# Performance work log

Hardware: AMD Instinct MI355X
Metric: run time of the kernel (lower is better)

Reference implementation:

```python
import jax, jax.numpy as jnp
from jax import lax
import numpy as np

N = 4
ALPHA_AP = 0.85
ALPHA_DS = 0.1
ALPHA_LR = 1.0
C1 = 0.01 ** 2
C2 = 0.03 ** 2


def resize_ac(img, nh, nw):
    # bilinear resize, align_corners=True (matches F.interpolate(..., align_corners=True))
    B, C, H, W = img.shape
    ys = jnp.linspace(0.0, H - 1.0, nh)
    xs = jnp.linspace(0.0, W - 1.0, nw)
    y0 = jnp.floor(ys).astype(jnp.int32)
    y1 = jnp.minimum(y0 + 1, H - 1)
    x0 = jnp.floor(xs).astype(jnp.int32)
    x1 = jnp.minimum(x0 + 1, W - 1)
    wy = (ys - y0).astype(img.dtype)[None, None, :, None]
    wx = (xs - x0).astype(img.dtype)[None, None, None, :]
    top = img[:, :, y0, :] * (1.0 - wy) + img[:, :, y1, :] * wy
    return top[:, :, :, x0] * (1.0 - wx) + top[:, :, :, x1] * wx


def build_pyramid(img):
    B, C, H, W = img.shape
    pyr = [img]
    for i in range(N - 1):
        r = 2 ** (i + 1)
        pyr.append(resize_ac(pyr[i], H // r, W // r))  # resize previous level, as in torch code
    return pyr


def x_grad(img):
    # replicate-pad right then diff -> last column is exactly zero
    g = img[:, :, :, :-1] - img[:, :, :, 1:]
    return jnp.concatenate([g, jnp.zeros_like(img[:, :, :, :1])], axis=3)


def y_grad(img):
    g = img[:, :, :-1, :] - img[:, :, 1:, :]
    return jnp.concatenate([g, jnp.zeros_like(img[:, :, :1, :])], axis=2)


def avgpool3(x):
    # AvgPool2d(3, 1), VALID padding
    return lax.reduce_window(x, 0.0, lax.add, (1, 1, 3, 3), (1, 1, 1, 1), 'VALID') / 9.0


def grid_sample_zeros(img, gx, gy):
    # bilinear grid_sample, padding_mode='zeros', align_corners=True
    B, C, H, W = img.shape
    x = (gx + 1.0) * 0.5 * (W - 1)
    y = (gy + 1.0) * 0.5 * (H - 1)
    x0 = jnp.floor(x)
    y0 = jnp.floor(y)

    def corner(xi, yi, w):
        valid = (xi >= 0) & (xi <= W - 1) & (yi >= 0) & (yi <= H - 1)
        xc = jnp.clip(xi, 0, W - 1).astype(jnp.int32)
        yc = jnp.clip(yi, 0, H - 1).astype(jnp.int32)
        vals = jax.vmap(lambda im, yy, xx: im[:, yy, xx])(img, yc, xc)  # [B,C,H,W]
        return vals * (w * valid.astype(img.dtype))[:, None]

    return (corner(x0, y0, (x0 + 1 - x) * (y0 + 1 - y))
            + corner(x0 + 1, y0, (x - x0) * (y0 + 1 - y))
            + corner(x0, y0 + 1, (x0 + 1 - x) * (y - y0))
            + corner(x0 + 1, y0 + 1, (x - x0) * (y - y0)))


def apply_disparity(img, disp):
    # standard Monodepth bilinear sampler: shift x_base in [0,1] by disp, grid_sample
    B, C, H, W = img.shape
    x_base = jnp.linspace(0.0, 1.0, W)[None, None, :]
    y_base = jnp.linspace(0.0, 1.0, H)[None, :, None]
    gx = 2.0 * (x_base + disp[:, 0]) - 1.0  # [B,H,W]
    gy = jnp.broadcast_to(2.0 * y_base - 1.0, gx.shape)
    return grid_sample_zeros(img, gx, gy)


def dssim(x, y):
    mu_x = avgpool3(x)
    mu_y = avgpool3(y)
    sig_x = avgpool3(x * x) - mu_x ** 2
    sig_y = avgpool3(y * y) - mu_y ** 2
    cov = avgpool3(x * y) - mu_x * mu_y
    ssim = ((2.0 * mu_x * mu_y + C1) * (2.0 * cov + C2)) / ((mu_x ** 2 + mu_y ** 2 + C1) * (sig_x + sig_y + C2))
    return jnp.mean(jnp.clip((1.0 - ssim) / 2.0, 0.0, 1.0))


def smoothness(disp, img, level):
    wx = jnp.exp(-jnp.mean(jnp.abs(x_grad(img)), axis=1, keepdims=True))
    wy = jnp.exp(-jnp.mean(jnp.abs(y_grad(img)), axis=1, keepdims=True))
    sx = x_grad(disp) * wx
    sy = y_grad(disp) * wy
    return jnp.mean(jnp.abs(sx) + jnp.abs(sy)) / (2 ** level)


def loss_forward(disps, left, right):
    lp = build_pyramid(left)
    rp = build_pyramid(right)
    dl = [d[:, 0:1] for d in disps]
    dr = [d[:, 1:2] for d in disps]
    left_est = [apply_disparity(rp[i], -dl[i]) for i in range(N)]
    right_est = [apply_disparity(lp[i], dr[i]) for i in range(N)]
    r2l_disp = [apply_disparity(dr[i], -dl[i]) for i in range(N)]
    l2r_disp = [apply_disparity(dl[i], dr[i]) for i in range(N)]
    # appearance matching (note: outer *ALPHA_AP matches the original's AP_loss*self.alpha_AP)
    AP = sum(ALPHA_AP * dssim(lp[i], left_est[i]) + (1.0 - ALPHA_AP) * jnp.mean(jnp.abs(lp[i] - left_est[i])) for i in range(N))
    AP = AP + sum(ALPHA_AP * dssim(rp[i], right_est[i]) + (1.0 - ALPHA_AP) * jnp.mean(jnp.abs(rp[i] - right_est[i])) for i in range(N))
    AP = AP * ALPHA_AP
    LR = sum(jnp.mean(jnp.abs(dl[i] - r2l_disp[i])) for i in range(N))
    LR = (LR + sum(jnp.mean(jnp.abs(dr[i] - l2r_disp[i])) for i in range(N))) * ALPHA_LR
    DS = sum(smoothness(dl[i], lp[i], i) for i in range(N))
    DS = (DS + sum(smoothness(dr[i], rp[i], i) for i in range(N))) * ALPHA_DS
    total = AP + LR + DS
    return total, AP, LR, DS


def setup_inputs() -> dict:
    key = jax.random.key(0)
    ks = jax.random.split(key, 6)
    B, H, W = 32, 256, 512
    inp = {}
    for i in range(N):
        h, w = H >> i, W >> i
        # normalized disparities in [0, 0.05) as in trained Monodepth
        inp[f'disp{i}'] = jax.random.uniform(ks[i], (B, 2, h, w), jnp.float32) * 0.05
    inp['left'] = jax.random.uniform(ks[4], (B, 3, H, W), jnp.float32)
    inp['right'] = jax.random.uniform(ks[5], (B, 3, H, W), jnp.float32)
    return inp


def reference(disp0, disp1, disp2, disp3, left, right):
    return loss_forward([disp0, disp1, disp2, disp3], left, right)
```

## Files before the change

### kernel.cpp

```cpp
#include <hip/hip_runtime.h>

#define BDIM 256
#define SH 16

struct LevelDesc {
    const float* lp; const float* rp; const float* dp;
    int H, W, nCW, nRS, nPerSide, waveBase;
};
struct AllParams { LevelDesc lv[4]; int totalWaves; };

__global__ void zero_acc_kernel(double* acc) {
    if (threadIdx.x < 32) acc[threadIdx.x] = 0.0;
}

__global__ void resize2_kernel(const float* __restrict__ sL, const float* __restrict__ sR,
                               float* __restrict__ dL, float* __restrict__ dR,
                               int BC, int Hs, int Ws, int Hd, int Wd) {
    long long half = (long long)BC * Hd * Wd;
    long long idx = (long long)blockIdx.x * blockDim.x + threadIdx.x;
    if (idx >= 2 * half) return;
    const float* src = (idx < half) ? sL : sR;
    float* dst = (idx < half) ? dL : dR;
    long long id = (idx < half) ? idx : idx - half;
    int i = (int)(id % Wd);
    long long t = id / Wd;
    int j = (int)(t % Hd);
    int bc = (int)(t / Hd);
    float stepy = (float)(Hs - 1) / (float)(Hd - 1);
    float stepx = (float)(Ws - 1) / (float)(Wd - 1);
    float y = j * stepy;
    float x = i * stepx;
    int y0 = (int)floorf(y);
    int y1 = min(y0 + 1, Hs - 1);
    int x0 = (int)floorf(x);
    int x1 = min(x0 + 1, Ws - 1);
    float wy = y - (float)y0;
    float wx = x - (float)x0;
    const float* s = src + (long long)bc * Hs * Ws;
    float t0 = s[(long long)y0 * Ws + x0] * (1.0f - wy) + s[(long long)y1 * Ws + x0] * wy;
    float t1 = s[(long long)y0 * Ws + x1] * (1.0f - wy) + s[(long long)y1 * Ws + x1] * wy;
    dst[id] = t0 * (1.0f - wx) + t1 * wx;
}

__device__ __forceinline__ float ssim_term(float Sx, float Sy, float Sxx, float Syy, float Sxy) {
    const float C1v = 0.0001f;
    const float C2v = 0.0009f;
    float mux = Sx * (1.0f / 9.0f), muy = Sy * (1.0f / 9.0f);
    float sigx = Sxx * (1.0f / 9.0f) - mux * mux;
    float sigy = Syy * (1.0f / 9.0f) - muy * muy;
    float cov  = Sxy * (1.0f / 9.0f) - mux * muy;
    float num = (2.0f * mux * muy + C1v) * (2.0f * cov + C2v);
    float den = (mux * mux + muy * muy + C1v) * (sigx + sigy + C2v);
    float v = (1.0f - num * __builtin_amdgcn_rcpf(den)) * 0.5f;
    return fminf(fmaxf(v, 0.0f), 1.0f);
}

__global__ void __launch_bounds__(BDIM)
mega_kernel(AllParams P, double* __restrict__ acc) {
    const int lane = threadIdx.x & 63;
    const int wid  = threadIdx.x >> 6;
    const int wId  = blockIdx.x * (BDIM / 64) + wid;
    const int w = min(wId, P.totalWaves - 1);

    int level = 0;
    if (w >= P.lv[1].waveBase) level = 1;
    if (w >= P.lv[2].waveBase) level = 2;
    if (w >= P.lv[3].waveBase) level = 3;
    LevelDesc L;
    if (level == 0) L = P.lv[0];
    else if (level == 1) L = P.lv[1];
    else if (level == 2) L = P.lv[2];
    else L = P.lv[3];

    int rel = w - L.waveBase;
    const int side = (rel >= L.nPerSide) ? 1 : 0;
    rel -= side * L.nPerSide;
    const int cw = rel % L.nCW; rel /= L.nCW;
    const int rs = rel % L.nRS;
    const int b  = rel / L.nRS;

    const int H = L.H, W = L.W;
    const long long HW = (long long)H * W;
    const float Wm1f = (float)(W - 1);
    const float sgn = side ? 1.0f : -1.0f;

    const float* xim = (side ? L.rp : L.lp) + (long long)b * 3 * HW;
    const float* sim = (side ? L.lp : L.rp) + (long long)b * 3 * HW;
    const float* dme = L.dp + (long long)b * 2 * HW + (side ? HW : 0);
    const float* dot = L.dp + (long long)b * 2 * HW + (side ? 0 : HW);

    const int base = cw * 126;
    const int c0 = base + 2 * lane;
    const int c1 = c0 + 1;
    const bool in0 = c0 < W, in1 = c1 < W;
    const int cc = min(c0, W - 2) >> 1;
    const float fc0 = (float)c0, fc1 = (float)c1;

    const bool lastW = (cw == L.nCW - 1);
    const bool own0 = in0 && (c0 < base + 126 || lastW);
    const bool own1 = in1 && (c1 < base + 126 || lastW);
    const bool ownS0 = own0 && (c0 <= W - 3);
    const bool ownS1 = own1 && (c1 <= W - 3);

    const int r0 = rs * SH;
    const int r1 = min(r0 + SH, H);
    const int jend = min(r1 + 1, H - 1);

    float Pst[3][5][2], Lst[3][5][2];
#pragma unroll
    for (int c = 0; c < 3; ++c)
#pragma unroll
        for (int s = 0; s < 5; ++s) { Pst[c][s][0] = 0.f; Pst[c][s][1] = 0.f;
                                      Lst[c][s][0] = 0.f; Lst[c][s][1] = 0.f; }
    float pd0 = 0.f, pd1 = 0.f;
    float pxv[3][2] = {{0.f,0.f},{0.f,0.f},{0.f,0.f}};

    float f_ss = 0.f, f_l1 = 0.f, f_lr = 0.f, f_ds = 0.f;

    for (int j = r0; j <= jend; ++j) {
        const long long ro = (long long)j * W;
        float2 dpair = ((const float2*)(dme + ro))[cc];
        float d0 = dpair.x, d1 = dpair.y;

        float xq0 = fmaf(sgn * d0, Wm1f, fc0);
        float xq1 = fmaf(sgn * d1, Wm1f, fc1);
        float xf0 = floorf(xq0), xf1 = floorf(xq1);
        int g0 = (int)xf0, g1 = (int)xf1;
        float t0 = xq0 - xf0, t1 = xq1 - xf1;
        float w00 = (g0 >= 0 && g0 < W)         ? 1.0f - t0 : 0.0f;
        float w01 = (g0 >= -1 && g0 < W - 1)    ? t0        : 0.0f;
        float w10 = (g1 >= 0 && g1 < W)         ? 1.0f - t1 : 0.0f;
        float w11 = (g1 >= -1 && g1 < W - 1)    ? t1        : 0.0f;
        int a0 = min(max(g0, 0), W - 1);
        int a1 = min(max(g0 + 1, 0), W - 1);
        int b0 = min(max(g1, 0), W - 1);
        int b1 = min(max(g1 + 1, 0), W - 1);

        const float* dor = dot + ro;
        float wv0 = dor[a0] * w00 + dor[a1] * w01;
        float wv1 = dor[b0] * w10 + dor[b1] * w11;

        float xv[3][2], yv[3][2];
#pragma unroll
        for (int c = 0; c < 3; ++c) {
            const float* xr = xim + (long long)c * HW + ro;
            const float* sr = sim + (long long)c * HW + ro;
            float2 xp2 = ((const float2*)xr)[cc];
            xv[c][0] = in0 ? xp2.x : 0.f;
            xv[c][1] = in1 ? xp2.y : 0.f;
            yv[c][0] = sr[a0] * w00 + sr[a1] * w01;
            yv[c][1] = sr[b0] * w10 + sr[b1] * w11;
            if (!in0) yv[c][0] = 0.f;
            if (!in1) yv[c][1] = 0.f;
        }

        const bool rowOwn = j < r1;
        if (rowOwn) {
            if (own0) {
                f_l1 += fabsf(xv[0][0] - yv[0][0]) + fabsf(xv[1][0] - yv[1][0]) + fabsf(xv[2][0] - yv[2][0]);
                f_lr += fabsf(d0 - wv0);
            }
            if (own1) {
                f_l1 += fabsf(xv[0][1] - yv[0][1]) + fabsf(xv[1][1] - yv[1][1]) + fabsf(xv[2][1] - yv[2][1]);
                f_lr += fabsf(d1 - wv1);
            }
        }

        {
            float dn  = __shfl_down(d0, 1);
            float xn0 = __shfl_down(xv[0][0], 1);
            float xn1 = __shfl_down(xv[1][0], 1);
            float xn2 = __shfl_down(xv[2][0], 1);
            if (rowOwn) {
                if (own0 && c0 < W - 1) {
                    float g = fabsf(xv[0][0] - xv[0][1]) + fabsf(xv[1][0] - xv[1][1]) + fabsf(xv[2][0] - xv[2][1]);
                    f_ds += fabsf((d0 - d1) * __expf(-g * (1.0f / 3.0f)));
                }
                if (own1 && c1 < W - 1) {
                    float g = fabsf(xv[0][1] - xn0) + fabsf(xv[1][1] - xn1) + fabsf(xv[2][1] - xn2);
                    f_ds += fabsf((d1 - dn) * __expf(-g * (1.0f / 3.0f)));
                }
            }
        }
        if (j > r0 && (j - 1) < r1) {
            if (own0) {
                float g = fabsf(pxv[0][0] - xv[0][0]) + fabsf(pxv[1][0] - xv[1][0]) + fabsf(pxv[2][0] - xv[2][0]);
                f_ds += fabsf((pd0 - d0) * __expf(-g * (1.0f / 3.0f)));
            }
            if (own1) {
                float g = fabsf(pxv[0][1] - xv[0][1]) + fabsf(pxv[1][1] - xv[1][1]) + fabsf(pxv[2][1] - xv[2][1]);
                f_ds += fabsf((pd1 - d1) * __expf(-g * (1.0f / 3.0f)));
            }
        }
        pd0 = d0; pd1 = d1;
#pragma unroll
        for (int c = 0; c < 3; ++c) { pxv[c][0] = xv[c][0]; pxv[c][1] = xv[c][1]; }

        const bool emit = (j >= r0 + 2);
#pragma unroll
        for (int c = 0; c < 3; ++c) {
            float cs[5][2];
#pragma unroll
            for (int p = 0; p < 2; ++p) {
                float cx = xv[c][p], cy = yv[c][p];
                float v5[5] = {cx, cy, cx * cx, cy * cy, cx * cy};
#pragma unroll
                for (int s = 0; s < 5; ++s) {
                    cs[s][p] = Pst[c][s][p] + v5[s];
                    Pst[c][s][p] = Lst[c][s][p] + v5[s];
                    Lst[c][s][p] = v5[s];
                }
            }
            if (emit) {
                float w0s[5], w1s[5];
#pragma unroll
                for (int s = 0; s < 5; ++s) {
                    float n0 = __shfl_down(cs[s][0], 1);
                    float n1 = __shfl_down(cs[s][1], 1);
                    w0s[s] = cs[s][0] + cs[s][1] + n0;
                    w1s[s] = cs[s][1] + n0 + n1;
                }
                float ts0 = ssim_term(w0s[0], w0s[1], w0s[2], w0s[3], w0s[4]);
                float ts1 = ssim_term(w1s[0], w1s[1], w1s[2], w1s[3], w1s[4]);
                f_ss += (ownS0 ? ts0 : 0.f) + (ownS1 ? ts1 : 0.f);
            }
        }
    }

#pragma unroll
    for (int o = 32; o > 0; o >>= 1) {
        f_ss += __shfl_down(f_ss, o);
        f_l1 += __shfl_down(f_l1, o);
        f_lr += __shfl_down(f_lr, o);
        f_ds += __shfl_down(f_ds, o);
    }
    __shared__ float red[BDIM / 64][4];
    __shared__ int meta[2];
    if (threadIdx.x == 0) { meta[0] = level; meta[1] = side; }
    if (lane == 0) {
        red[wid][0] = f_ss; red[wid][1] = f_l1;
        red[wid][2] = f_lr; red[wid][3] = f_ds;
    }
    __syncthreads();
    if (threadIdx.x < 4) {
        int t = threadIdx.x;
        double s = (double)red[0][t] + (double)red[1][t]
                 + (double)red[2][t] + (double)red[3][t];
        atomicAdd(acc + t * 8 + meta[1] * 4 + meta[0], s);
    }
}

__global__ void finalize_kernel(const double* __restrict__ acc, float* __restrict__ out) {
    const int B = 32, H0 = 256, W0 = 512;
    double AP = 0.0, LR = 0.0, DS = 0.0;
    for (int i = 0; i < 4; ++i) {
        int h = H0 >> i, w = W0 >> i;
        double nss = (double)B * 3.0 * (double)(h - 2) * (double)(w - 2);
        double nl1 = (double)B * 3.0 * (double)h * (double)w;
        double nd  = (double)B * (double)h * (double)w;
        AP += 0.85 * (acc[0 + i] / nss) + 0.15 * (acc[8 + i] / nl1);
        AP += 0.85 * (acc[4 + i] / nss) + 0.15 * (acc[12 + i] / nl1);
        LR += acc[16 + i] / nd + acc[20 + i] / nd;
        double sc = 1.0 / (double)(1 << i);
        DS += (acc[24 + i] / nd) * sc + (acc[28 + i] / nd) * sc;
    }
    AP *= 0.85;
    DS *= 0.1;
    double total = AP + LR + DS;
    out[0] = (float)total;
    out[1] = (float)AP;
    out[2] = (float)LR;
    out[3] = (float)DS;
}

extern "C" void kernel_launch(void* const* d_in, const int* in_sizes, int n_in,
                              void* d_out, int out_size, void* d_ws, size_t ws_size,
                              hipStream_t stream) {
    const int B = 32, H0 = 256, W0 = 512;
    const float* dsp[4];
    for (int i = 0; i < 4; ++i) dsp[i] = (const float*)d_in[i];
    const float* left  = (const float*)d_in[4];
    const float* right = (const float*)d_in[5];
    float* out = (float*)d_out;

    double* acc = (double*)d_ws;
    float* buf = (float*)((char*)d_ws + 256);

    const float* lp[4];
    const float* rp[4];
    float* lpm[4];
    float* rpm[4];
    lp[0] = left; rp[0] = right;
    float* cur = buf;
    for (int i = 1; i < 4; ++i) { lpm[i] = cur; cur += (long long)B * 3 * (H0 >> i) * (W0 >> i); }
    for (int i = 1; i < 4; ++i) { rpm[i] = cur; cur += (long long)B * 3 * (H0 >> i) * (W0 >> i); }
    for (int i = 1; i < 4; ++i) { lp[i] = lpm[i]; rp[i] = rpm[i]; }

    zero_acc_kernel<<<1, 64, 0, stream>>>(acc);

    for (int i = 1; i < 4; ++i) {
        int Hs = H0 >> (i - 1), Ws = W0 >> (i - 1);
        int Hd = H0 >> i, Wd = W0 >> i;
        long long half = (long long)B * 3 * Hd * Wd;
        int g = (int)((2 * half + BDIM - 1) / BDIM);
        resize2_kernel<<<g, BDIM, 0, stream>>>(
            lp[i - 1], rp[i - 1], lpm[i], rpm[i], B * 3, Hs, Ws, Hd, Wd);
    }

    AllParams P;
    int wb = 0;
    for (int i = 0; i < 4; ++i) {
        int h = H0 >> i, w = W0 >> i;
        LevelDesc& L = P.lv[i];
        L.lp = lp[i]; L.rp = rp[i]; L.dp = dsp[i];
        L.H = h; L.W = w;
        L.nCW = (w - 2 + 125) / 126;
        L.nRS = h / SH;
        L.nPerSide = B * L.nRS * L.nCW;
        L.waveBase = wb;
        wb += 2 * L.nPerSide;
    }
    P.totalWaves = wb;
    int blocks = (wb + (BDIM / 64) - 1) / (BDIM / 64);
    mega_kernel<<<blocks, BDIM, 0, stream>>>(P, acc);

    finalize_kernel<<<1, 1, 0, stream>>>(acc, out);
}
```

Before: 301.7 us.

## Fuse resize, loss and finalize into one persistent kernel with grid barriers

Merges the three pyramid resize launches, the main loss kernel and the finalize kernel into a single persistent kernel of 1280 blocks. Stages are separated by atomic-counter grid barriers. The row split per wave is rebalanced so each wave handles H/nChunks rows, with exactly 5120 waves. This removes launch overhead and tail effects, but relies on all 1280 blocks being co-resident (launch bounds request 5 blocks per CU), otherwise the spin barrier deadlocks. It also hardcodes the wave partition per level.

```diff
diff --git a/kernel.cpp b/kernel.cpp
--- a/kernel.cpp
+++ b/kernel.cpp
@@ -1,45 +1,63 @@
 #include <hip/hip_runtime.h>
 
 #define BDIM 256
-#define SH 16
+#define GRID 1280
+#define NWAVES (GRID * (BDIM / 64))
 
 struct LevelDesc {
     const float* lp; const float* rp; const float* dp;
-    int H, W, nCW, nRS, nPerSide, waveBase;
+    int H, W, nCW, nChunks, base, nPerSide;
 };
-struct AllParams { LevelDesc lv[4]; int totalWaves; };
-
-__global__ void zero_acc_kernel(double* acc) {
+struct Params {
+    LevelDesc lv[4];
+    const float* left; const float* right;
+    float* l1; float* r1; float* l2; float* r2; float* l3; float* r3;
+    double* acc; unsigned int* cnt; float* out;
+};
+
+__global__ void init_kernel(double* acc, unsigned int* cnt) {
     if (threadIdx.x < 32) acc[threadIdx.x] = 0.0;
-}
-
-__global__ void resize2_kernel(const float* __restrict__ sL, const float* __restrict__ sR,
-                               float* __restrict__ dL, float* __restrict__ dR,
-                               int BC, int Hs, int Ws, int Hd, int Wd) {
-    long long half = (long long)BC * Hd * Wd;
-    long long idx = (long long)blockIdx.x * blockDim.x + threadIdx.x;
-    if (idx >= 2 * half) return;
-    const float* src = (idx < half) ? sL : sR;
-    float* dst = (idx < half) ? dL : dR;
-    long long id = (idx < half) ? idx : idx - half;
-    int i = (int)(id % Wd);
-    long long t = id / Wd;
-    int j = (int)(t % Hd);
-    int bc = (int)(t / Hd);
-    float stepy = (float)(Hs - 1) / (float)(Hd - 1);
-    float stepx = (float)(Ws - 1) / (float)(Wd - 1);
-    float y = j * stepy;
-    float x = i * stepx;
-    int y0 = (int)floorf(y);
-    int y1 = min(y0 + 1, Hs - 1);
-    int x0 = (int)floorf(x);
-    int x1 = min(x0 + 1, Ws - 1);
-    float wy = y - (float)y0;
-    float wx = x - (float)x0;
-    const float* s = src + (long long)bc * Hs * Ws;
-    float t0 = s[(long long)y0 * Ws + x0] * (1.0f - wy) + s[(long long)y1 * Ws + x0] * wy;
-    float t1 = s[(long long)y0 * Ws + x1] * (1.0f - wy) + s[(long long)y1 * Ws + x1] * wy;
-    dst[id] = t0 * (1.0f - wx) + t1 * wx;
+    else if (threadIdx.x == 32) *cnt = 0u;
+}
+
+__device__ __forceinline__ void gsync(unsigned int* cnt, unsigned int target) {
+    __syncthreads();
+    if (threadIdx.x == 0) {
+        __threadfence();
+        atomicAdd(cnt, 1u);
+        while (atomicAdd(cnt, 0u) < target) __builtin_amdgcn_s_sleep(2);
+        __threadfence();
+    }
+    __syncthreads();
+}
+
+__device__ void resize_dev(const float* __restrict__ sL, const float* __restrict__ sR,
+                           float* __restrict__ dL, float* __restrict__ dR,
+                           int BC, int Hs, int Ws, int Hd, int Wd, int tid, int nt) {
+    const long long half = (long long)BC * Hd * Wd;
+    const float stepy = (float)(Hs - 1) / (float)(Hd - 1);
+    const float stepx = (float)(Ws - 1) / (float)(Wd - 1);
+    for (long long idx = tid; idx < 2 * half; idx += nt) {
+        const float* src = (idx < half) ? sL : sR;
+        float* dst = (idx < half) ? dL : dR;
+        long long id = (idx < half) ? idx : idx - half;
+        int i = (int)(id % Wd);
+        long long t = id / Wd;
+        int j = (int)(t % Hd);
+        int bc = (int)(t / Hd);
+        float y = j * stepy;
+        float x = i * stepx;
+        int y0 = (int)floorf(y);
+        int y1 = min(y0 + 1, Hs - 1);
+        int x0 = (int)floorf(x);
+        int x1 = min(x0 + 1, Ws - 1);
+        float wy = y - (float)y0;
+        float wx = x - (float)x0;
+        const float* s = src + (long long)bc * Hs * Ws;
+        float t0 = s[(long long)y0 * Ws + x0] * (1.0f - wy) + s[(long long)y1 * Ws + x0] * wy;
+        float t1 = s[(long long)y0 * Ws + x1] * (1.0f - wy) + s[(long long)y1 * Ws + x1] * wy;
+        dst[id] = t0 * (1.0f - wx) + t1 * wx;
+    }
 }
 
 __device__ __forceinline__ float ssim_term(float Sx, float Sy, float Sxx, float Syy, float Sxy) {
@@ -55,29 +73,28 @@
     return fminf(fmaxf(v, 0.0f), 1.0f);
 }
 
-__global__ void __launch_bounds__(BDIM)
-mega_kernel(AllParams P, double* __restrict__ acc) {
+__device__ void mega_dev(const Params& P) {
     const int lane = threadIdx.x & 63;
     const int wid  = threadIdx.x >> 6;
-    const int wId  = blockIdx.x * (BDIM / 64) + wid;
-    const int w = min(wId, P.totalWaves - 1);
+    const int w    = blockIdx.x * (BDIM / 64) + wid;
 
     int level = 0;
-    if (w >= P.lv[1].waveBase) level = 1;
-    if (w >= P.lv[2].waveBase) level = 2;
-    if (w >= P.lv[3].waveBase) level = 3;
+    if (w >= P.lv[1].base) level = 1;
+    if (w >= P.lv[2].base) level = 2;
+    if (w >= P.lv[3].base) level = 3;
     LevelDesc L;
     if (level == 0) L = P.lv[0];
     else if (level == 1) L = P.lv[1];
     else if (level == 2) L = P.lv[2];
     else L = P.lv[3];
 
-    int rel = w - L.waveBase;
+    int rel = w - L.base;
     const int side = (rel >= L.nPerSide) ? 1 : 0;
     rel -= side * L.nPerSide;
-    const int cw = rel % L.nCW; rel /= L.nCW;
-    const int rs = rel % L.nRS;
-    const int b  = rel / L.nRS;
+    const int chunk = rel % L.nChunks;
+    const int r3i = rel / L.nChunks;
+    const int cw = r3i % L.nCW;
+    const int b  = r3i / L.nCW;
 
     const int H = L.H, W = L.W;
     const long long HW = (long long)H * W;
@@ -102,8 +119,8 @@
     const bool ownS0 = own0 && (c0 <= W - 3);
     const bool ownS1 = own1 && (c1 <= W - 3);
 
-    const int r0 = rs * SH;
-    const int r1 = min(r0 + SH, H);
+    const int r0 = (chunk * H) / L.nChunks;
+    const int r1 = ((chunk + 1) * H) / L.nChunks;
     const int jend = min(r1 + 1, H - 1);
 
     float Pst[3][5][2], Lst[3][5][2];
@@ -127,10 +144,10 @@
         float xf0 = floorf(xq0), xf1 = floorf(xq1);
         int g0 = (int)xf0, g1 = (int)xf1;
         float t0 = xq0 - xf0, t1 = xq1 - xf1;
-        float w00 = (g0 >= 0 && g0 < W)         ? 1.0f - t0 : 0.0f;
-        float w01 = (g0 >= -1 && g0 < W - 1)    ? t0        : 0.0f;
-        float w10 = (g1 >= 0 && g1 < W)         ? 1.0f - t1 : 0.0f;
-        float w11 = (g1 >= -1 && g1 < W - 1)    ? t1        : 0.0f;
+        float w00 = (g0 >= 0 && g0 < W)      ? 1.0f - t0 : 0.0f;
+        float w01 = (g0 >= -1 && g0 < W - 1) ? t0        : 0.0f;
+        float w10 = (g1 >= 0 && g1 < W)      ? 1.0f - t1 : 0.0f;
+        float w11 = (g1 >= -1 && g1 < W - 1) ? t1        : 0.0f;
         int a0 = min(max(g0, 0), W - 1);
         int a1 = min(max(g0 + 1, 0), W - 1);
         int b0 = min(max(g1, 0), W - 1);
@@ -246,83 +263,79 @@
         int t = threadIdx.x;
         double s = (double)red[0][t] + (double)red[1][t]
                  + (double)red[2][t] + (double)red[3][t];
-        atomicAdd(acc + t * 8 + meta[1] * 4 + meta[0], s);
-    }
-}
-
-__global__ void finalize_kernel(const double* __restrict__ acc, float* __restrict__ out) {
+        atomicAdd(P.acc + t * 8 + meta[1] * 4 + meta[0], s);
+    }
+    __syncthreads();
+}
+
+__device__ void finalize_dev(double* acc, float* out) {
     const int B = 32, H0 = 256, W0 = 512;
+    double a[32];
+    for (int i = 0; i < 32; ++i) a[i] = atomicAdd(acc + i, 0.0);
     double AP = 0.0, LR = 0.0, DS = 0.0;
     for (int i = 0; i < 4; ++i) {
         int h = H0 >> i, w = W0 >> i;
         double nss = (double)B * 3.0 * (double)(h - 2) * (double)(w - 2);
         double nl1 = (double)B * 3.0 * (double)h * (double)w;
         double nd  = (double)B * (double)h * (double)w;
-        AP += 0.85 * (acc[0 + i] / nss) + 0.15 * (acc[8 + i] / nl1);
-        AP += 0.85 * (acc[4 + i] / nss) + 0.15 * (acc[12 + i] / nl1);
-        LR += acc[16 + i] / nd + acc[20 + i] / nd;
+        AP += 0.85 * (a[0 + i] / nss) + 0.15 * (a[8 + i] / nl1);
+        AP += 0.85 * (a[4 + i] / nss) + 0.15 * (a[12 + i] / nl1);
+        LR += a[16 + i] / nd + a[20 + i] / nd;
         double sc = 1.0 / (double)(1 << i);
-        DS += (acc[24 + i] / nd) * sc + (acc[28 + i] / nd) * sc;
+        DS += (a[24 + i] / nd) * sc + (a[28 + i] / nd) * sc;
     }
     AP *= 0.85;
     DS *= 0.1;
-    double total = AP + LR + DS;
-    out[0] = (float)total;
+    out[0] = (float)(AP + LR + DS);
     out[1] = (float)AP;
     out[2] = (float)LR;
     out[3] = (float)DS;
 }
 
+__global__ void __launch_bounds__(BDIM, 5)
+everything_kernel(Params P) {
+    const int tid = blockIdx.x * BDIM + threadIdx.x;
+    const int nt = GRID * BDIM;
+    resize_dev(P.left, P.right, P.l1, P.r1, 96, 256, 512, 128, 256, tid, nt);
+    gsync(P.cnt, 1u * GRID);
+    resize_dev(P.l1, P.r1, P.l2, P.r2, 96, 128, 256, 64, 128, tid, nt);
+    gsync(P.cnt, 2u * GRID);
+    resize_dev(P.l2, P.r2, P.l3, P.r3, 96, 64, 128, 32, 64, tid, nt);
+    gsync(P.cnt, 3u * GRID);
+    mega_dev(P);
+    gsync(P.cnt, 4u * GRID);
+    if (tid == 0) finalize_dev(P.acc, P.out);
+}
+
 extern "C" void kernel_launch(void* const* d_in, const int* in_sizes, int n_in,
                               void* d_out, int out_size, void* d_ws, size_t ws_size,
                               hipStream_t stream) {
-    const int B = 32, H0 = 256, W0 = 512;
+    const int B = 32;
     const float* dsp[4];
     for (int i = 0; i < 4; ++i) dsp[i] = (const float*)d_in[i];
     const float* left  = (const float*)d_in[4];
     const float* right = (const float*)d_in[5];
-    float* out = (float*)d_out;
 
     double* acc = (double*)d_ws;
-    float* buf = (float*)((char*)d_ws + 256);
-
-    const float* lp[4];
-    const float* rp[4];
-    float* lpm[4];
-    float* rpm[4];
-    lp[0] = left; rp[0] = right;
+    unsigned int* cnt = (unsigned int*)((char*)d_ws + 256);
+    float* buf = (float*)((char*)d_ws + 512);
+
+    Params P;
+    P.left = left; P.right = right;
+    P.acc = acc; P.cnt = cnt; P.out = (float*)d_out;
     float* cur = buf;
-    for (int i = 1; i < 4; ++i) { lpm[i] = cur; cur += (long long)B * 3 * (H0 >> i) * (W0 >> i); }
-    for (int i = 1; i < 4; ++i) { rpm[i] = cur; cur += (long long)B * 3 * (H0 >> i) * (W0 >> i); }
-    for (int i = 1; i < 4; ++i) { lp[i] = lpm[i]; rp[i] = rpm[i]; }
-
-    zero_acc_kernel<<<1, 64, 0, stream>>>(acc);
-
-    for (int i = 1; i < 4; ++i) {
-        int Hs = H0 >> (i - 1), Ws = W0 >> (i - 1);
-        int Hd = H0 >> i, Wd = W0 >> i;
-        long long half = (long long)B * 3 * Hd * Wd;
-        int g = (int)((2 * half + BDIM - 1) / BDIM);
-        resize2_kernel<<<g, BDIM, 0, stream>>>(
-            lp[i - 1], rp[i - 1], lpm[i], rpm[i], B * 3, Hs, Ws, Hd, Wd);
-    }
-
-    AllParams P;
-    int wb = 0;
-    for (int i = 0; i < 4; ++i) {
-        int h = H0 >> i, w = W0 >> i;
-        LevelDesc& L = P.lv[i];
-        L.lp = lp[i]; L.rp = rp[i]; L.dp = dsp[i];
-        L.H = h; L.W = w;
-        L.nCW = (w - 2 + 125) / 126;
-        L.nRS = h / SH;
-        L.nPerSide = B * L.nRS * L.nCW;
-        L.waveBase = wb;
-        wb += 2 * L.nPerSide;
-    }
-    P.totalWaves = wb;
-    int blocks = (wb + (BDIM / 64) - 1) / (BDIM / 64);
-    mega_kernel<<<blocks, BDIM, 0, stream>>>(P, acc);
-
-    finalize_kernel<<<1, 1, 0, stream>>>(acc, out);
-}
+    P.l1 = cur; cur += (long long)B * 3 * 128 * 256;
+    P.r1 = cur; cur += (long long)B * 3 * 128 * 256;
+    P.l2 = cur; cur += (long long)B * 3 * 64 * 128;
+    P.r2 = cur; cur += (long long)B * 3 * 64 * 128;
+    P.l3 = cur; cur += (long long)B * 3 * 32 * 64;
+    P.r3 = cur; cur += (long long)B * 3 * 32 * 64;
+
+    P.lv[0] = { left,  right, dsp[0], 256, 512, 5, 11,    0, 1760 };
+    P.lv[1] = { P.l1,  P.r1,  dsp[1], 128, 256, 3,  6, 3520,  576 };
+    P.lv[2] = { P.l2,  P.r2,  dsp[2],  64, 128, 1,  4, 4672,  128 };
+    P.lv[3] = { P.l3,  P.r3,  dsp[3],  32,  64, 1,  3, 4928,   96 };
+
+    init_kernel<<<1, 64, 0, stream>>>(acc, cnt);
+    everything_kernel<<<GRID, BDIM, 0, stream>>>(P);
+}
```

Result: slower. 1.199 ms (+297.5%).
